# Kernel tuning notes

Measured on AMD Instinct MI355X. Metric: run time of the kernel, lower is better.

## Reference

```python
import jax, jax.numpy as jnp
import numpy as np
import math

B, T, C, H = 2, 2048, 1024, 16


def setup_inputs() -> dict:
    key = jax.random.key(0)
    k1, k2, k3 = jax.random.split(key, 3)
    x = jax.random.normal(k1, (B, T, C), dtype=jnp.float32)
    qkv_w = jax.random.normal(k2, (3 * C, C), dtype=jnp.float32) * 0.02
    proj_w = jax.random.normal(k3, (C, C), dtype=jnp.float32) * 0.02
    distance_scales = jnp.full((H,), 0.1, dtype=jnp.float32)
    return {"x": x, "qkv_w": qkv_w, "proj_w": proj_w, "distance_scales": distance_scales}


def reference(x, qkv_w, proj_w, distance_scales):
    b, t, c = x.shape
    h = distance_scales.shape[0]
    dh = c // h
    scale = 1.0 / math.sqrt(dh)

    # torch Linear: y = x @ W^T ; split into q, k, v
    qkv = jnp.einsum('btc,oc->bto', x, qkv_w)  # [B,T,3C]
    q, k, v = jnp.split(qkv, 3, axis=-1)
    q = q.reshape(b, t, h, dh).transpose(0, 2, 1, 3)  # [B,H,T,Dh]
    k = k.reshape(b, t, h, dh).transpose(0, 2, 1, 3)
    v = v.reshape(b, t, h, dh).transpose(0, 2, 1, 3)

    logits = jnp.einsum('bhid,bhjd->bhij', q, k) * scale  # [B,H,T,T]

    idx = jnp.arange(t)
    dists = jnp.abs(idx[:, None] - idx[None, :]).astype(x.dtype)  # [T,T]
    logits = logits - distance_scales[None, :, None, None] * dists

    causal = idx[None, :] > idx[:, None]  # True above diagonal -> masked
    logits = jnp.where(causal[None, None, :, :], -jnp.inf, logits)

    attn = jax.nn.softmax(logits, axis=-1)  # [B,H,T,T]

    dist_energy = (attn * dists).sum(axis=-1).mean()
    flop_energy = -(attn * jnp.log(attn + 1e-9)).sum(axis=-1).mean()

    out = jnp.einsum('bhij,bhjd->bhid', attn, v)  # [B,H,T,Dh]
    out = out.transpose(0, 2, 1, 3).reshape(b, t, c)
    out = jnp.einsum('btc,oc->bto', out, proj_w)

    return (out, dist_energy, flop_energy, jax.lax.stop_gradient(attn), jax.lax.stop_gradient(dists))
```

## Files before the change

### kernel.cpp

```cpp
#include <hip/hip_runtime.h>
#include <hip/hip_bf16.h>
#include <math.h>

#define T_SEQ 2048
#define NH 16
#define C3 3072
#define C_DIM 1024

typedef __bf16 bf16_t;
typedef __bf16 bf16x8 __attribute__((ext_vector_type(8)));
typedef __bf16 bf16x4_t __attribute__((ext_vector_type(4)));
typedef float f32x4 __attribute__((ext_vector_type(4)));

static __device__ __forceinline__ bf16x8 ldfrag(const bf16_t* p) {
    return *reinterpret_cast<const bf16x8*>(p);
}

__global__ void cvt4_kernel(const float* __restrict__ in, bf16_t* __restrict__ out,
                            long n4, float* zbuf) {
    long i = (long)blockIdx.x * blockDim.x + threadIdx.x;
    if (zbuf && i < 2) zbuf[i] = 0.f;
    long stride = (long)gridDim.x * blockDim.x;
    for (; i < n4; i += stride) {
        float4 v = ((const float4*)in)[i];
        bf16x4_t o;
        o[0] = (bf16_t)v.x; o[1] = (bf16_t)v.y; o[2] = (bf16_t)v.z; o[3] = (bf16_t)v.w;
        *(bf16x4_t*)(out + i * 4) = o;
    }
}

__global__ void dists_kernel(float* __restrict__ dout) {
    int idx = blockIdx.x * 256 + threadIdx.x;
    int i = idx >> 11, j = idx & 2047;
    dout[idx] = (float)(i > j ? i - j : j - i);
}

template <bool OUT_BF16>
__global__ __launch_bounds__(256) void gemm_bt(const bf16_t* __restrict__ A,
                                               const bf16_t* __restrict__ Bw,
                                               void* __restrict__ Cout,
                                               int M, int N, int K) {
    __shared__ bf16_t sA[128][72];
    __shared__ bf16_t sB[128][72];
    int tid = threadIdx.x;
    int lane = tid & 63, wid = tid >> 6;
    int m = lane & 15, quad = lane >> 4;
    int wm = (wid >> 1) * 64, wn = (wid & 1) * 64;
    int m0 = blockIdx.y * 128, n0 = blockIdx.x * 128;
    int r0 = tid >> 3, c8 = (tid & 7) << 3;

    f32x4 acc[4][4] = {};
    for (int k0 = 0; k0 < K; k0 += 64) {
        for (int p = 0; p < 4; ++p) {
            int row = r0 + p * 32;
            *(uint4*)&sA[row][c8] = *(const uint4*)&A[(size_t)(m0 + row) * K + k0 + c8];
            *(uint4*)&sB[row][c8] = *(const uint4*)&Bw[(size_t)(n0 + row) * K + k0 + c8];
        }
        __syncthreads();
        for (int ks = 0; ks < 64; ks += 32) {
            bf16x8 a[4], b[4];
            for (int i = 0; i < 4; ++i) a[i] = ldfrag(&sA[wm + i * 16 + m][ks + quad * 8]);
            for (int i = 0; i < 4; ++i) b[i] = ldfrag(&sB[wn + i * 16 + m][ks + quad * 8]);
            for (int i = 0; i < 4; ++i)
                for (int j = 0; j < 4; ++j)
                    acc[i][j] = __builtin_amdgcn_mfma_f32_16x16x32_bf16(a[i], b[j], acc[i][j], 0, 0, 0);
        }
        __syncthreads();
    }
    for (int i = 0; i < 4; ++i)
        for (int j = 0; j < 4; ++j)
            for (int r = 0; r < 4; ++r) {
                int row = m0 + wm + i * 16 + quad * 4 + r;
                int col = n0 + wn + j * 16 + m;
                float v = acc[i][j][r];
                if (OUT_BF16) ((bf16_t*)Cout)[(size_t)row * N + col] = (bf16_t)v;
                else          ((float*)Cout)[(size_t)row * N + col] = v;
            }
}

__global__ __launch_bounds__(256) void repack_vt(const bf16_t* __restrict__ qkv,
                                                 bf16_t* __restrict__ vt) {
    __shared__ bf16_t s[64][72];
    int t0 = (blockIdx.x & 31) << 6;
    int bh = blockIdx.x >> 5;
    int b = bh >> 4, h = bh & 15;
    int tid = threadIdx.x;
    int r = tid >> 3, c8 = (tid & 7) << 3;
    const bf16_t* src = qkv + (size_t)(b * T_SEQ) * C3 + 2048 + h * 64;
    for (int p = 0; p < 2; ++p) {
        int t = r + p * 32;
        *(uint4*)&s[t][c8] = *(const uint4*)&src[(size_t)(t0 + t) * C3 + c8];
    }
    __syncthreads();
    bf16_t* dst = vt + (size_t)bh * 64 * T_SEQ;
    for (int p = 0; p < 2; ++p) {
        int d = r + p * 32;
        bf16x8 vv;
        for (int i = 0; i < 8; ++i) vv[i] = s[c8 + i][d];
        *(bf16x8*)&dst[(size_t)d * T_SEQ + t0 + c8] = vv;
    }
}

__global__ __launch_bounds__(256) void attn_kernel(const bf16_t* __restrict__ qkv,
                                                   const bf16_t* __restrict__ vt,
                                                   const float* __restrict__ dscales,
                                                   float* __restrict__ attn,
                                                   bf16_t* __restrict__ y,
                                                   float* __restrict__ ews) {
    __shared__ bf16_t sQ[64][72], sK[64][72], sV[64][72], sP[64][72];
    __shared__ float sred[8];
    int base = blockIdx.x & 31;
    int bh = (blockIdx.x >> 5) & 31;
    int it = (bh & 8) ? (31 - base) : base;
    int b = bh >> 4, h = bh & 15;
    int i0 = it << 6;
    int tid = threadIdx.x, lane = tid & 63, wid = tid >> 6;
    int m = lane & 15, quad = lane >> 4;
    int w16 = wid << 4;
    float dsc = dscales[h];
    const float scale = 0.125f;

    const bf16_t* Qb = qkv + (size_t)(b * T_SEQ) * C3 + h * 64;
    const bf16_t* Kb = Qb + 1024;
    const bf16_t* Vb = vt + (size_t)bh * 64 * T_SEQ;
    float* Ab = attn + ((size_t)bh * T_SEQ + i0) * T_SEQ;

    {
        int zc0 = i0 + 64;
        for (int r = 0; r < 64; ++r) {
            float* rowp = Ab + (size_t)r * T_SEQ;
            for (int c = zc0 + (tid << 1); c < T_SEQ; c += 512)
                *(float2*)(rowp + c) = make_float2(0.f, 0.f);
        }
    }

    int r0 = tid >> 3, c8 = (tid & 7) << 3;
    for (int p = 0; p < 2; ++p) {
        int r = r0 + p * 32;
        *(uint4*)&sQ[r][c8] = *(const uint4*)&Qb[(size_t)(i0 + r) * C3 + c8];
    }

    float mrow[4], lrow[4];
    for (int r = 0; r < 4; ++r) { mrow[r] = -3.0e38f; lrow[r] = 0.f; }

    for (int jt = 0; jt <= it; ++jt) {
        int j0 = jt << 6;
        __syncthreads();
        for (int p = 0; p < 2; ++p) {
            int rr = r0 + p * 32;
            *(uint4*)&sK[rr][c8] = *(const uint4*)&Kb[(size_t)(j0 + rr) * C3 + c8];
        }
        __syncthreads();
        f32x4 acc[4] = {};
        for (int ks = 0; ks < 64; ks += 32) {
            bf16x8 a = ldfrag(&sQ[w16 + m][ks + quad * 8]);
            for (int n = 0; n < 4; ++n) {
                bf16x8 bb = ldfrag(&sK[n * 16 + m][ks + quad * 8]);
                acc[n] = __builtin_amdgcn_mfma_f32_16x16x32_bf16(a, bb, acc[n], 0, 0, 0);
            }
        }
        for (int r = 0; r < 4; ++r) {
            int gi = i0 + w16 + quad * 4 + r;
            float s4[4];
            float mx = -3.0e38f;
            for (int n = 0; n < 4; ++n) {
                int gj = j0 + n * 16 + m;
                float s = acc[n][r] * scale - dsc * fabsf((float)(gi - gj));
                if (gj > gi) s = -3.0e38f;
                s4[n] = s;
                mx = fmaxf(mx, s);
            }
            for (int off = 1; off < 16; off <<= 1) mx = fmaxf(mx, __shfl_xor(mx, off));
            float mnew = fmaxf(mrow[r], mx);
            float se = 0.f;
            for (int n = 0; n < 4; ++n) se += __expf(s4[n] - mnew);
            for (int off = 1; off < 16; off <<= 1) se += __shfl_xor(se, off);
            lrow[r] = lrow[r] * __expf(mrow[r] - mnew) + se;
            mrow[r] = mnew;
        }
    }

    float rl[4];
    for (int r = 0; r < 4; ++r) rl[r] = 1.f / lrow[r];
    f32x4 oacc[4] = {};
    float e_d = 0.f, e_e = 0.f;

    for (int jt = 0; jt <= it; ++jt) {
        int j0 = jt << 6;
        __syncthreads();
        for (int p = 0; p < 2; ++p) {
            int rr = r0 + p * 32;
            *(uint4*)&sK[rr][c8] = *(const uint4*)&Kb[(size_t)(j0 + rr) * C3 + c8];
            *(uint4*)&sV[rr][c8] = *(const uint4*)&Vb[(size_t)rr * T_SEQ + j0 + c8];
        }
        __syncthreads();
        f32x4 acc[4] = {};
        for (int ks = 0; ks < 64; ks += 32) {
            bf16x8 a = ldfrag(&sQ[w16 + m][ks + quad * 8]);
            for (int n = 0; n < 4; ++n) {
                bf16x8 bb = ldfrag(&sK[n * 16 + m][ks + quad * 8]);
                acc[n] = __builtin_amdgcn_mfma_f32_16x16x32_bf16(a, bb, acc[n], 0, 0, 0);
            }
        }
        for (int r = 0; r < 4; ++r) {
            int gi = i0 + w16 + quad * 4 + r;
            float* rowp = Ab + (size_t)(w16 + quad * 4 + r) * T_SEQ + j0;
            for (int n = 0; n < 4; ++n) {
                int gj = j0 + n * 16 + m;
                float d = fabsf((float)(gi - gj));
                float s = acc[n][r] * scale - dsc * d;
                if (gj > gi) s = -3.0e38f;
                float p = __expf(s - mrow[r]) * rl[r];
                rowp[n * 16 + m] = p;
                e_d += p * d;
                e_e += p * __logf(p + 1e-9f);
                sP[w16 + quad * 4 + r][n * 16 + m] = (bf16_t)p;
            }
        }
        __syncthreads();
        for (int ks = 0; ks < 64; ks += 32) {
            bf16x8 a = ldfrag(&sP[w16 + m][ks + quad * 8]);
            for (int n = 0; n < 4; ++n) {
                bf16x8 bb = ldfrag(&sV[n * 16 + m][ks + quad * 8]);
                oacc[n] = __builtin_amdgcn_mfma_f32_16x16x32_bf16(a, bb, oacc[n], 0, 0, 0);
            }
        }
    }

    for (int n = 0; n < 4; ++n)
        for (int r = 0; r < 4; ++r) {
            int t = i0 + w16 + quad * 4 + r;
            y[(size_t)(b * T_SEQ + t) * C_DIM + h * 64 + n * 16 + m] = (bf16_t)oacc[n][r];
        }

    for (int off = 1; off < 64; off <<= 1) {
        e_d += __shfl_xor(e_d, off);
        e_e += __shfl_xor(e_e, off);
    }
    if (lane == 0) { sred[wid] = e_d; sred[wid + 4] = e_e; }
    __syncthreads();
    if (tid == 0) {
        atomicAdd(ews, sred[0] + sred[1] + sred[2] + sred[3]);
        atomicAdd(ews + 1, sred[4] + sred[5] + sred[6] + sred[7]);
    }
}

__global__ void finalize_kernel(const float* __restrict__ ews, float* __restrict__ dout) {
    dout[4194304] = ews[0] / 65536.f;
    dout[4194305] = -ews[1] / 65536.f;
}

extern "C" void kernel_launch(void* const* d_in, const int* in_sizes, int n_in,
                              void* d_out, int out_size, void* d_ws, size_t ws_size,
                              hipStream_t stream) {
    const float* x = (const float*)d_in[0];
    const float* qkv_w = (const float*)d_in[1];
    const float* proj_w = (const float*)d_in[2];
    const float* dscales = (const float*)d_in[3];
    float* out = (float*)d_out;

    char* ws = (char*)d_ws;
    float* ews   = (float*)ws;
    bf16_t* xb   = (bf16_t*)(ws + 256);
    bf16_t* wb   = xb + 4194304;
    bf16_t* pb   = wb + 3145728;
    bf16_t* qkvb = pb + 1048576;
    bf16_t* vtb  = qkvb + 12582912;
    bf16_t* yb   = vtb + 4194304;

    cvt4_kernel<<<1024, 256, 0, stream>>>(x, xb, 4194304 / 4, ews);
    cvt4_kernel<<<1024, 256, 0, stream>>>(qkv_w, wb, 3145728 / 4, nullptr);
    cvt4_kernel<<<512, 256, 0, stream>>>(proj_w, pb, 1048576 / 4, nullptr);
    dists_kernel<<<16384, 256, 0, stream>>>(out + 138412034);

    gemm_bt<true><<<dim3(24, 32), 256, 0, stream>>>(xb, wb, qkvb, 4096, 3072, 1024);
    repack_vt<<<1024, 256, 0, stream>>>(qkvb, vtb);
    attn_kernel<<<1024, 256, 0, stream>>>(qkvb, vtb, dscales, out + 4194306, yb, ews);
    gemm_bt<false><<<dim3(8, 32), 256, 0, stream>>>(yb, pb, out, 4096, 1024, 1024);
    finalize_kernel<<<1, 1, 0, stream>>>(ews, out);
}
```

Measured before the change: 915.5 us.

## Rework GEMM with direct-to-LDS swizzled loads and restructure attention without max pass

Result: faster. 873.2 us (-4.6%).

```diff
diff --git a/kernel.cpp b/kernel.cpp
--- a/kernel.cpp
+++ b/kernel.cpp
@@ -3,7 +3,6 @@
 #include <math.h>
 
 #define T_SEQ 2048
-#define NH 16
 #define C3 3072
 #define C_DIM 1024
 
@@ -12,7 +11,10 @@
 typedef __bf16 bf16x4_t __attribute__((ext_vector_type(4)));
 typedef float f32x4 __attribute__((ext_vector_type(4)));
 
-static __device__ __forceinline__ bf16x8 ldfrag(const bf16_t* p) {
+typedef __attribute__((address_space(1))) const void gconst_t;
+typedef __attribute__((address_space(3))) void lds_t;
+
+static __device__ __forceinline__ bf16x8 ldg8(const bf16_t* p) {
     return *reinterpret_cast<const bf16x8*>(p);
 }
 
@@ -35,47 +37,61 @@
     dout[idx] = (float)(i > j ? i - j : j - i);
 }
 
-template <bool OUT_BF16>
+template <int BM, bool OUT_BF16>
 __global__ __launch_bounds__(256) void gemm_bt(const bf16_t* __restrict__ A,
                                                const bf16_t* __restrict__ Bw,
                                                void* __restrict__ Cout,
                                                int M, int N, int K) {
-    __shared__ bf16_t sA[128][72];
-    __shared__ bf16_t sB[128][72];
-    int tid = threadIdx.x;
-    int lane = tid & 63, wid = tid >> 6;
+    constexpr int WM = BM / 2;
+    constexpr int MI = WM / 16;
+    __shared__ bf16_t sA[BM * 64];
+    __shared__ bf16_t sB[128 * 64];
+    int tid = threadIdx.x, lane = tid & 63, wid = tid >> 6;
     int m = lane & 15, quad = lane >> 4;
-    int wm = (wid >> 1) * 64, wn = (wid & 1) * 64;
-    int m0 = blockIdx.y * 128, n0 = blockIdx.x * 128;
-    int r0 = tid >> 3, c8 = (tid & 7) << 3;
-
-    f32x4 acc[4][4] = {};
+    int wm = (wid >> 1) * WM, wn = (wid & 1) * 64;
+    int m0 = blockIdx.y * BM, n0 = blockIdx.x * 128;
+    int lrow = lane >> 3, cxor = (lane & 7) ^ (lrow & 7);
+
+    const bf16_t* Ag = A + (size_t)(m0 + wid * 8 + lrow) * K + cxor * 8;
+    const bf16_t* Bg = Bw + (size_t)(n0 + wid * 8 + lrow) * K + cxor * 8;
+
+    f32x4 acc[MI][4] = {};
     for (int k0 = 0; k0 < K; k0 += 64) {
-        for (int p = 0; p < 4; ++p) {
-            int row = r0 + p * 32;
-            *(uint4*)&sA[row][c8] = *(const uint4*)&A[(size_t)(m0 + row) * K + k0 + c8];
-            *(uint4*)&sB[row][c8] = *(const uint4*)&Bw[(size_t)(n0 + row) * K + k0 + c8];
-        }
-        __syncthreads();
-        for (int ks = 0; ks < 64; ks += 32) {
-            bf16x8 a[4], b[4];
-            for (int i = 0; i < 4; ++i) a[i] = ldfrag(&sA[wm + i * 16 + m][ks + quad * 8]);
-            for (int i = 0; i < 4; ++i) b[i] = ldfrag(&sB[wn + i * 16 + m][ks + quad * 8]);
-            for (int i = 0; i < 4; ++i)
+        for (int p = 0; p < BM / 32; ++p)
+            __builtin_amdgcn_global_load_lds((gconst_t*)(Ag + (size_t)(p * 32) * K + k0),
+                                             (lds_t*)(sA + (p * 32 + wid * 8) * 64), 16, 0, 0);
+        for (int p = 0; p < 4; ++p)
+            __builtin_amdgcn_global_load_lds((gconst_t*)(Bg + (size_t)(p * 32) * K + k0),
+                                             (lds_t*)(sB + (p * 32 + wid * 8) * 64), 16, 0, 0);
+        __syncthreads();
+        for (int ks = 0; ks < 2; ++ks) {
+            bf16x8 a[MI], b[4];
+            for (int i = 0; i < MI; ++i) {
+                int r = wm + i * 16 + m;
+                a[i] = *(const bf16x8*)(sA + r * 64 + ((((ks << 2) + quad) ^ (r & 7)) << 3));
+            }
+            for (int j = 0; j < 4; ++j) {
+                int r = wn + j * 16 + m;
+                b[j] = *(const bf16x8*)(sB + r * 64 + ((((ks << 2) + quad) ^ (r & 7)) << 3));
+            }
+            for (int i = 0; i < MI; ++i)
                 for (int j = 0; j < 4; ++j)
-                    acc[i][j] = __builtin_amdgcn_mfma_f32_16x16x32_bf16(a[i], b[j], acc[i][j], 0, 0, 0);
-        }
-        __syncthreads();
-    }
-    for (int i = 0; i < 4; ++i)
-        for (int j = 0; j < 4; ++j)
-            for (int r = 0; r < 4; ++r) {
-                int row = m0 + wm + i * 16 + quad * 4 + r;
-                int col = n0 + wn + j * 16 + m;
-                float v = acc[i][j][r];
-                if (OUT_BF16) ((bf16_t*)Cout)[(size_t)row * N + col] = (bf16_t)v;
-                else          ((float*)Cout)[(size_t)row * N + col] = v;
-            }
+                    acc[i][j] = __builtin_amdgcn_mfma_f32_16x16x32_bf16(b[j], a[i], acc[i][j], 0, 0, 0);
+        }
+        __syncthreads();
+    }
+    for (int i = 0; i < MI; ++i)
+        for (int j = 0; j < 4; ++j) {
+            size_t row = m0 + wm + i * 16 + m;
+            int col = n0 + wn + j * 16 + quad * 4;
+            if (OUT_BF16) {
+                bf16x4_t o;
+                for (int r = 0; r < 4; ++r) o[r] = (bf16_t)acc[i][j][r];
+                *(bf16x4_t*)((bf16_t*)Cout + row * N + col) = o;
+            } else {
+                *(f32x4*)((float*)Cout + row * N + col) = acc[i][j];
+            }
+        }
 }
 
 __global__ __launch_bounds__(256) void repack_vt(const bf16_t* __restrict__ qkv,
@@ -107,10 +123,10 @@
                                                    float* __restrict__ attn,
                                                    bf16_t* __restrict__ y,
                                                    float* __restrict__ ews) {
-    __shared__ bf16_t sQ[64][72], sK[64][72], sV[64][72], sP[64][72];
+    __shared__ bf16_t sP[64][72];
     __shared__ float sred[8];
     int base = blockIdx.x & 31;
-    int bh = (blockIdx.x >> 5) & 31;
+    int bh = blockIdx.x >> 5;
     int it = (bh & 8) ? (31 - base) : base;
     int b = bh >> 4, h = bh & 15;
     int i0 = it << 6;
@@ -119,6 +135,7 @@
     int w16 = wid << 4;
     float dsc = dscales[h];
     const float scale = 0.125f;
+    const float zthr = 111.0f;
 
     const bf16_t* Qb = qkv + (size_t)(b * T_SEQ) * C3 + h * 64;
     const bf16_t* Kb = Qb + 1024;
@@ -126,112 +143,101 @@
     float* Ab = attn + ((size_t)bh * T_SEQ + i0) * T_SEQ;
 
     {
-        int zc0 = i0 + 64;
+        int zc0 = i0 + 64, zn = T_SEQ - zc0;
+        f32x4 z4 = {0.f, 0.f, 0.f, 0.f};
         for (int r = 0; r < 64; ++r) {
-            float* rowp = Ab + (size_t)r * T_SEQ;
-            for (int c = zc0 + (tid << 1); c < T_SEQ; c += 512)
-                *(float2*)(rowp + c) = make_float2(0.f, 0.f);
-        }
-    }
-
-    int r0 = tid >> 3, c8 = (tid & 7) << 3;
-    for (int p = 0; p < 2; ++p) {
-        int r = r0 + p * 32;
-        *(uint4*)&sQ[r][c8] = *(const uint4*)&Qb[(size_t)(i0 + r) * C3 + c8];
-    }
-
-    float mrow[4], lrow[4];
-    for (int r = 0; r < 4; ++r) { mrow[r] = -3.0e38f; lrow[r] = 0.f; }
-
+            float* rowp = Ab + (size_t)r * T_SEQ + zc0;
+            for (int c = tid << 2; c < zn; c += 1024)
+                *(f32x4*)(rowp + c) = z4;
+        }
+    }
+
+    int i = i0 + w16 + m;
+    bf16x8 qf[2];
+    qf[0] = ldg8(Qb + (size_t)i * C3 + quad * 8);
+    qf[1] = ldg8(Qb + (size_t)i * C3 + 32 + quad * 8);
+
+    float lsum = 0.f;
     for (int jt = 0; jt <= it; ++jt) {
         int j0 = jt << 6;
-        __syncthreads();
-        for (int p = 0; p < 2; ++p) {
-            int rr = r0 + p * 32;
-            *(uint4*)&sK[rr][c8] = *(const uint4*)&Kb[(size_t)(j0 + rr) * C3 + c8];
-        }
-        __syncthreads();
+        if ((float)(i0 - j0 - 63) * dsc > zthr) continue;
         f32x4 acc[4] = {};
-        for (int ks = 0; ks < 64; ks += 32) {
-            bf16x8 a = ldfrag(&sQ[w16 + m][ks + quad * 8]);
+        for (int ks = 0; ks < 2; ++ks)
             for (int n = 0; n < 4; ++n) {
-                bf16x8 bb = ldfrag(&sK[n * 16 + m][ks + quad * 8]);
-                acc[n] = __builtin_amdgcn_mfma_f32_16x16x32_bf16(a, bb, acc[n], 0, 0, 0);
-            }
-        }
-        for (int r = 0; r < 4; ++r) {
-            int gi = i0 + w16 + quad * 4 + r;
-            float s4[4];
-            float mx = -3.0e38f;
-            for (int n = 0; n < 4; ++n) {
-                int gj = j0 + n * 16 + m;
-                float s = acc[n][r] * scale - dsc * fabsf((float)(gi - gj));
-                if (gj > gi) s = -3.0e38f;
-                s4[n] = s;
-                mx = fmaxf(mx, s);
-            }
-            for (int off = 1; off < 16; off <<= 1) mx = fmaxf(mx, __shfl_xor(mx, off));
-            float mnew = fmaxf(mrow[r], mx);
-            float se = 0.f;
-            for (int n = 0; n < 4; ++n) se += __expf(s4[n] - mnew);
-            for (int off = 1; off < 16; off <<= 1) se += __shfl_xor(se, off);
-            lrow[r] = lrow[r] * __expf(mrow[r] - mnew) + se;
-            mrow[r] = mnew;
-        }
-    }
-
-    float rl[4];
-    for (int r = 0; r < 4; ++r) rl[r] = 1.f / lrow[r];
+                bf16x8 kf = ldg8(Kb + (size_t)(j0 + n * 16 + m) * C3 + ks * 32 + quad * 8);
+                acc[n] = __builtin_amdgcn_mfma_f32_16x16x32_bf16(kf, qf[ks], acc[n], 0, 0, 0);
+            }
+        if (jt < it) {
+            for (int n = 0; n < 4; ++n)
+                for (int r = 0; r < 4; ++r) {
+                    float d = (float)(i - (j0 + n * 16 + quad * 4 + r));
+                    lsum += __expf(acc[n][r] * scale - dsc * d);
+                }
+        } else {
+            for (int n = 0; n < 4; ++n)
+                for (int r = 0; r < 4; ++r) {
+                    int j = j0 + n * 16 + quad * 4 + r;
+                    if (j <= i) lsum += __expf(acc[n][r] * scale - dsc * (float)(i - j));
+                }
+        }
+    }
+    lsum += __shfl_xor(lsum, 16);
+    lsum += __shfl_xor(lsum, 32);
+    float rl = 1.f / lsum;
+
     f32x4 oacc[4] = {};
     float e_d = 0.f, e_e = 0.f;
 
     for (int jt = 0; jt <= it; ++jt) {
         int j0 = jt << 6;
-        __syncthreads();
-        for (int p = 0; p < 2; ++p) {
-            int rr = r0 + p * 32;
-            *(uint4*)&sK[rr][c8] = *(const uint4*)&Kb[(size_t)(j0 + rr) * C3 + c8];
-            *(uint4*)&sV[rr][c8] = *(const uint4*)&Vb[(size_t)rr * T_SEQ + j0 + c8];
-        }
-        __syncthreads();
+        if ((float)(i0 - j0 - 63) * dsc > zthr) {
+            int rr = tid >> 2, c0 = (tid & 3) << 4;
+            float* p0 = Ab + (size_t)rr * T_SEQ + j0 + c0;
+            f32x4 z4 = {0.f, 0.f, 0.f, 0.f};
+            for (int u = 0; u < 4; ++u) *(f32x4*)(p0 + u * 4) = z4;
+            continue;
+        }
         f32x4 acc[4] = {};
-        for (int ks = 0; ks < 64; ks += 32) {
-            bf16x8 a = ldfrag(&sQ[w16 + m][ks + quad * 8]);
+        for (int ks = 0; ks < 2; ++ks)
             for (int n = 0; n < 4; ++n) {
-                bf16x8 bb = ldfrag(&sK[n * 16 + m][ks + quad * 8]);
-                acc[n] = __builtin_amdgcn_mfma_f32_16x16x32_bf16(a, bb, acc[n], 0, 0, 0);
-            }
-        }
-        for (int r = 0; r < 4; ++r) {
-            int gi = i0 + w16 + quad * 4 + r;
-            float* rowp = Ab + (size_t)(w16 + quad * 4 + r) * T_SEQ + j0;
+                bf16x8 kf = ldg8(Kb + (size_t)(j0 + n * 16 + m) * C3 + ks * 32 + quad * 8);
+                acc[n] = __builtin_amdgcn_mfma_f32_16x16x32_bf16(kf, qf[ks], acc[n], 0, 0, 0);
+            }
+        __syncthreads();
+        bool diag = (jt == it);
+        for (int n = 0; n < 4; ++n) {
+            f32x4 pv;
+            for (int r = 0; r < 4; ++r) {
+                int j = j0 + n * 16 + quad * 4 + r;
+                float p = 0.f;
+                if (!diag || j <= i) {
+                    float d = (float)(i - j);
+                    p = __expf(acc[n][r] * scale - dsc * d) * rl;
+                    e_d += p * d;
+                    e_e += p * __logf(p + 1e-9f);
+                }
+                pv[r] = p;
+            }
+            *(f32x4*)(Ab + (size_t)(w16 + m) * T_SEQ + j0 + n * 16 + quad * 4) = pv;
+            bf16x4_t pb;
+            for (int r = 0; r < 4; ++r) pb[r] = (bf16_t)pv[r];
+            *(bf16x4_t*)&sP[w16 + m][n * 16 + quad * 4] = pb;
+        }
+        __syncthreads();
+        for (int ks = 0; ks < 2; ++ks) {
+            bf16x8 pf = *(const bf16x8*)&sP[w16 + m][ks * 32 + quad * 8];
             for (int n = 0; n < 4; ++n) {
-                int gj = j0 + n * 16 + m;
-                float d = fabsf((float)(gi - gj));
-                float s = acc[n][r] * scale - dsc * d;
-                if (gj > gi) s = -3.0e38f;
-                float p = __expf(s - mrow[r]) * rl[r];
-                rowp[n * 16 + m] = p;
-                e_d += p * d;
-                e_e += p * __logf(p + 1e-9f);
-                sP[w16 + quad * 4 + r][n * 16 + m] = (bf16_t)p;
-            }
-        }
-        __syncthreads();
-        for (int ks = 0; ks < 64; ks += 32) {
-            bf16x8 a = ldfrag(&sP[w16 + m][ks + quad * 8]);
-            for (int n = 0; n < 4; ++n) {
-                bf16x8 bb = ldfrag(&sV[n * 16 + m][ks + quad * 8]);
-                oacc[n] = __builtin_amdgcn_mfma_f32_16x16x32_bf16(a, bb, oacc[n], 0, 0, 0);
-            }
-        }
-    }
-
-    for (int n = 0; n < 4; ++n)
-        for (int r = 0; r < 4; ++r) {
-            int t = i0 + w16 + quad * 4 + r;
-            y[(size_t)(b * T_SEQ + t) * C_DIM + h * 64 + n * 16 + m] = (bf16_t)oacc[n][r];
-        }
+                bf16x8 vf = ldg8(Vb + (size_t)(n * 16 + m) * T_SEQ + j0 + ks * 32 + quad * 8);
+                oacc[n] = __builtin_amdgcn_mfma_f32_16x16x32_bf16(vf, pf, oacc[n], 0, 0, 0);
+            }
+        }
+    }
+
+    for (int n = 0; n < 4; ++n) {
+        bf16x4_t o;
+        for (int r = 0; r < 4; ++r) o[r] = (bf16_t)oacc[n][r];
+        *(bf16x4_t*)(y + (size_t)(b * T_SEQ + i) * C_DIM + h * 64 + n * 16 + quad * 4) = o;
+    }
 
     for (int off = 1; off < 64; off <<= 1) {
         e_d += __shfl_xor(e_d, off);
@@ -273,9 +279,9 @@
     cvt4_kernel<<<512, 256, 0, stream>>>(proj_w, pb, 1048576 / 4, nullptr);
     dists_kernel<<<16384, 256, 0, stream>>>(out + 138412034);
 
-    gemm_bt<true><<<dim3(24, 32), 256, 0, stream>>>(xb, wb, qkvb, 4096, 3072, 1024);
+    gemm_bt<128, true><<<dim3(24, 32), 256, 0, stream>>>(xb, wb, qkvb, 4096, 3072, 1024);
     repack_vt<<<1024, 256, 0, stream>>>(qkvb, vtb);
     attn_kernel<<<1024, 256, 0, stream>>>(qkvb, vtb, dscales, out + 4194306, yb, ews);
-    gemm_bt<false><<<dim3(8, 32), 256, 0, stream>>>(yb, pb, out, 4096, 1024, 1024);
+    gemm_bt<64, false><<<dim3(8, 64), 256, 0, stream>>>(yb, pb, out, 4096, 1024, 1024);
     finalize_kernel<<<1, 1, 0, stream>>>(ews, out);
 }
```
